# Kernel optimization log

Hardware: AMD Instinct MI355X
Metric: run time of the kernel (lower is better)

Reference implementation:

```python
import jax, jax.numpy as jnp
import numpy as np

HEADS = 16
EMBED = 1024
HEAD_DIM = EMBED // HEADS


def setup_inputs() -> dict:
    k = jax.random.key(0)
    ks = jax.random.split(k, 8)
    N, L = 8, 1024
    s = 1.0 / np.sqrt(HEAD_DIM)
    return {
        "key": jax.random.normal(ks[0], (N, L, EMBED), jnp.float32),
        "query": jax.random.normal(ks[1], (N, L, EMBED), jnp.float32),
        "value": jax.random.normal(ks[2], (N, L, EMBED), jnp.float32),
        "mask": jnp.ones((N, 1, 1, L), jnp.int32),
        "Wq": jax.random.normal(ks[3], (HEAD_DIM, HEAD_DIM), jnp.float32) * s,
        "Wk": jax.random.normal(ks[4], (HEAD_DIM, HEAD_DIM), jnp.float32) * s,
        "Wv": jax.random.normal(ks[5], (HEAD_DIM, HEAD_DIM), jnp.float32) * s,
        "Wo": jax.random.normal(ks[6], (EMBED, EMBED), jnp.float32) * (1.0 / np.sqrt(EMBED)),
    }


def reference(key, query, value, mask, Wq, Wk, Wv, Wo):
    # NOTE: original torch code calls weights.masked_fill(...) without assignment,
    # which is a no-op, so `mask` is faithfully ignored here.
    N, Lq, E = query.shape
    Lk = key.shape[1]
    H, D = HEADS, E // HEADS
    q = query.reshape(N, Lq, H, D)
    k = key.reshape(N, Lk, H, D)
    v = value.reshape(N, Lk, H, D)
    # per-head linear with weight shared across heads: x @ W^T (torch Linear)
    q = jnp.einsum('nqhd,ed->nqhe', q, Wq)
    k = jnp.einsum('nkhd,ed->nkhe', k, Wk)
    v = jnp.einsum('nkhd,ed->nkhe', v, Wv)
    weights = jnp.einsum('nqhd,nkhd->nhqk', q, k)
    attn = jax.nn.softmax(weights / jnp.sqrt(jnp.asarray(E, weights.dtype)), axis=-1)
    out = jnp.einsum('nhqk,nkhd->nqhd', attn, v).reshape(N, Lq, E)
    return out @ Wo.T
```

## Files before the change

kernel.cpp:

```cpp
#include <hip/hip_runtime.h>
#include <hip/hip_bf16.h>

#define HEADS 16
#define HDIM  64
#define EMB   1024
#define NB    8
#define SEQ   1024

typedef __bf16 bf16_t;
typedef __bf16 bf16x8 __attribute__((ext_vector_type(8)));
typedef __bf16 bf16x4 __attribute__((ext_vector_type(4)));
typedef float  floatx4 __attribute__((ext_vector_type(4)));
typedef float  f32x16  __attribute__((ext_vector_type(16)));
typedef unsigned uint2v __attribute__((ext_vector_type(2)));

union PkU { unsigned u; __bf16 h[2]; };
union W4U { unsigned u[4]; bf16x8 v; };

__device__ __forceinline__ bf16x8 load8bf(const bf16_t* p) { return *(const bf16x8*)p; }
__device__ __forceinline__ bf16x4 cvt4(float4 a) {
    bf16x4 r; r[0]=(bf16_t)a.x; r[1]=(bf16_t)a.y; r[2]=(bf16_t)a.z; r[3]=(bf16_t)a.w;
    return r;
}
__device__ __forceinline__ bf16x8 cvt8(float4 a, float4 b) {
    bf16x8 r;
    r[0]=(bf16_t)a.x; r[1]=(bf16_t)a.y; r[2]=(bf16_t)a.z; r[3]=(bf16_t)a.w;
    r[4]=(bf16_t)b.x; r[5]=(bf16_t)b.y; r[6]=(bf16_t)b.z; r[7]=(bf16_t)b.w;
    return r;
}

__global__ __launch_bounds__(256) void proj_kernel(
    const float* __restrict__ q_in, const float* __restrict__ k_in,
    const float* __restrict__ v_in,
    const float* __restrict__ Wq, const float* __restrict__ Wk,
    const float* __restrict__ Wv,
    bf16_t* __restrict__ qp, bf16_t* __restrict__ kp, bf16_t* __restrict__ vt)
{
    __shared__ __align__(16) bf16_t wl[64][72];
    __shared__ __align__(16) bf16_t lo[64][72];

    const int wave = threadIdx.x >> 6;
    const int lane = threadIdx.x & 63;
    const int m  = lane & 15;
    const int q4 = lane >> 4;
    const int op = blockIdx.y;

    const float* x = (op == 0) ? q_in : (op == 1) ? k_in : v_in;
    const float* W = (op == 0) ? Wq   : (op == 1) ? Wk   : Wv;

    {
        const int t  = threadIdx.x;
        const int f  = t >> 2;
        const int kg = (t & 3) * 16;
        #pragma unroll
        for (int j = 0; j < 4; ++j) {
            float4 v = *(const float4*)(W + f * 64 + kg + j * 4);
            *(bf16x4*)&wl[f][kg + j * 4] = cvt4(v);
        }
    }
    __syncthreads();

    if (op == 2) {
        const int nh = blockIdx.x >> 4;
        const int l0 = (blockIdx.x & 15) * 64;
        const int n  = nh >> 4;
        const int h  = nh & 15;

        const int la = l0 + wave * 16 + m;
        const float* xr = x + (size_t)(n * 16384 + la * 16 + h) * 64;
        float4 f0 = *(const float4*)(xr + q4 * 8);
        float4 f1 = *(const float4*)(xr + q4 * 8 + 4);
        float4 f2 = *(const float4*)(xr + 32 + q4 * 8);
        float4 f3 = *(const float4*)(xr + 32 + q4 * 8 + 4);
        bf16x8 a0 = cvt8(f0, f1);
        bf16x8 a1 = cvt8(f2, f3);

        floatx4 acc[4];
        #pragma unroll
        for (int sub = 0; sub < 4; ++sub) {
            bf16x8 b0 = load8bf(&wl[sub * 16 + m][q4 * 8]);
            bf16x8 b1 = load8bf(&wl[sub * 16 + m][32 + q4 * 8]);
            floatx4 z = {0.f, 0.f, 0.f, 0.f};
            z = __builtin_amdgcn_mfma_f32_16x16x32_bf16(a0, b0, z, 0, 0, 0);
            z = __builtin_amdgcn_mfma_f32_16x16x32_bf16(a1, b1, z, 0, 0, 0);
            acc[sub] = z;
        }

        #pragma unroll
        for (int sub = 0; sub < 4; ++sub) {
            #pragma unroll
            for (int r = 0; r < 4; r += 2) {
                PkU u; u.h[0] = (bf16_t)acc[sub][r]; u.h[1] = (bf16_t)acc[sub][r + 1];
                *(unsigned*)&lo[sub * 16 + m][wave * 16 + q4 * 4 + r] = u.u;
            }
        }
        __syncthreads();

        const int e  = threadIdx.x >> 2;
        const int lc = (threadIdx.x & 3) * 16;
        bf16_t* dst = vt + ((size_t)nh * 64 + e) * 1024 + l0 + lc;
        *(bf16x8*)dst       = *(const bf16x8*)&lo[e][lc];
        *(bf16x8*)(dst + 8) = *(const bf16x8*)&lo[e][lc + 8];
    } else {
        const float qscale = (op == 0) ? (1.4426950408889634f * 0.03125f) : 1.0f;
        const int row0 = blockIdx.x * 64 + wave * 16;

        const float* xr = x + (size_t)(row0 + m) * 64;
        float4 f0 = *(const float4*)(xr + q4 * 8);
        float4 f1 = *(const float4*)(xr + q4 * 8 + 4);
        float4 f2 = *(const float4*)(xr + 32 + q4 * 8);
        float4 f3 = *(const float4*)(xr + 32 + q4 * 8 + 4);
        bf16x8 a0 = cvt8(f0, f1);
        bf16x8 a1 = cvt8(f2, f3);

        floatx4 acc[4];
        #pragma unroll
        for (int sub = 0; sub < 4; ++sub) {
            bf16x8 b0 = load8bf(&wl[sub * 16 + m][q4 * 8]);
            bf16x8 b1 = load8bf(&wl[sub * 16 + m][32 + q4 * 8]);
            floatx4 z = {0.f, 0.f, 0.f, 0.f};
            z = __builtin_amdgcn_mfma_f32_16x16x32_bf16(a0, b0, z, 0, 0, 0);
            z = __builtin_amdgcn_mfma_f32_16x16x32_bf16(a1, b1, z, 0, 0, 0);
            acc[sub] = z;
        }

        #pragma unroll
        for (int sub = 0; sub < 4; ++sub) {
            #pragma unroll
            for (int r = 0; r < 4; ++r) {
                lo[wave * 16 + q4 * 4 + r][sub * 16 + m] = (bf16_t)(acc[sub][r] * qscale);
            }
        }
        __syncthreads();

        const int gl = threadIdx.x >> 2;
        const int ec = (threadIdx.x & 3) * 16;
        const int g  = blockIdx.x * 64 + gl;
        const int n  = g >> 14;
        const int l  = (g >> 4) & 1023;
        const int h  = g & 15;
        const int nh = n * 16 + h;
        bf16_t* dst = ((op == 0) ? qp : kp) + ((size_t)nh * 1024 + l) * 64 + ec;
        *(bf16x8*)dst       = *(const bf16x8*)&lo[gl][ec];
        *(bf16x8*)(dst + 8) = *(const bf16x8*)&lo[gl][ec + 8];
    }
}

__global__ __launch_bounds__(256) void attn_kernel(
    bf16_t* __restrict__ qp, const bf16_t* __restrict__ kp,
    const bf16_t* __restrict__ vt)
{
    __shared__ __align__(16) bf16_t kl[2][64][64];
    __shared__ __align__(16) bf16_t vl[2][64][64];

    const int lane = threadIdx.x & 63;
    const int wave = threadIdx.x >> 6;
    const int q32  = lane & 31;
    const int hi   = lane >> 5;

    const int nh   = blockIdx.x & 127;
    const int qblk = blockIdx.x >> 7;

    bf16_t* Q = qp + (size_t)nh * 65536;
    const bf16_t* K = kp + (size_t)nh * 65536;
    const bf16_t* V = vt + (size_t)nh * 65536;

    const int qb = qblk * 128 + wave * 32;

    const int srow  = lane >> 3;
    const int sslot = lane & 7;
    const int ch    = sslot ^ srow;

    auto stage = [&](int b, int kb) {
        #pragma unroll
        for (int i = 0; i < 2; ++i) {
            const int rbase = wave * 16 + i * 8;
            const int row   = rbase + srow;
            __builtin_amdgcn_global_load_lds(
                (const __attribute__((address_space(1))) unsigned int*)(K + (size_t)(kb + row) * 64 + ch * 8),
                (__attribute__((address_space(3))) unsigned int*)(&kl[b][rbase][0]),
                16, 0, 0);
            __builtin_amdgcn_global_load_lds(
                (const __attribute__((address_space(1))) unsigned int*)(V + (size_t)row * 1024 + kb + ch * 8),
                (__attribute__((address_space(3))) unsigned int*)(&vl[b][rbase][0]),
                16, 0, 0);
        }
    };

    stage(0, 0);

    bf16x8 bq[4];
    #pragma unroll
    for (int sl = 0; sl < 4; ++sl)
        bq[sl] = load8bf(Q + (size_t)(qb + q32) * 64 + sl * 16 + hi * 8);

    bf16x8 ones;
    #pragma unroll
    for (int j = 0; j < 8; ++j) ones[j] = (bf16_t)1.0f;

    f32x16 o0 = {0.f,0.f,0.f,0.f,0.f,0.f,0.f,0.f,0.f,0.f,0.f,0.f,0.f,0.f,0.f,0.f};
    f32x16 o1 = o0;
    f32x16 osum = o0;

    int cur = 0;
    __syncthreads();

    for (int kt = 0; kt < 16; ++kt) {
        if (kt < 15) stage(cur ^ 1, (kt + 1) * 64);

        #pragma unroll
        for (int kb32 = 0; kb32 < 2; ++kb32) {
            const int krow = kb32 * 32 + q32;
            f32x16 s = {0.f,0.f,0.f,0.f,0.f,0.f,0.f,0.f,0.f,0.f,0.f,0.f,0.f,0.f,0.f,0.f};
            __builtin_amdgcn_s_setprio(1);
            #pragma unroll
            for (int sl = 0; sl < 4; ++sl) {
                const int ck = ((sl * 2 + hi) ^ (krow & 7)) * 8;
                bf16x8 ka = load8bf(&kl[cur][krow][ck]);
                s = __builtin_amdgcn_mfma_f32_32x32x16_bf16(ka, bq[sl], s, 0, 0, 0);
            }
            __builtin_amdgcn_s_setprio(0);

            unsigned w[8];
            #pragma unroll
            for (int t = 0; t < 8; ++t) {
                float p0 = exp2f(s[2 * t]);
                float p1 = exp2f(s[2 * t + 1]);
                PkU u; u.h[0] = (bf16_t)p0; u.h[1] = (bf16_t)p1;
                w[t] = u.u;
            }

            bf16x8 va[4];
            #pragma unroll
            for (int db = 0; db < 2; ++db) {
                const int d = db * 32 + q32;
                #pragma unroll
                for (int c = 0; c < 2; ++c) {
                    const int cv = ((kb32 * 4 + c * 2 + hi) ^ (d & 7)) * 8;
                    va[db * 2 + c] = load8bf(&vl[cur][d][cv]);
                }
            }

            W4U b0v, b1v;
            uint2v r02 = __builtin_amdgcn_permlane32_swap(w[0], w[2], false, false);
            b0v.u[0] = r02[0]; b0v.u[2] = r02[1];
            uint2v r13 = __builtin_amdgcn_permlane32_swap(w[1], w[3], false, false);
            b0v.u[1] = r13[0]; b0v.u[3] = r13[1];
            uint2v r46 = __builtin_amdgcn_permlane32_swap(w[4], w[6], false, false);
            b1v.u[0] = r46[0]; b1v.u[2] = r46[1];
            uint2v r57 = __builtin_amdgcn_permlane32_swap(w[5], w[7], false, false);
            b1v.u[1] = r57[0]; b1v.u[3] = r57[1];

            __builtin_amdgcn_s_setprio(1);
            o0 = __builtin_amdgcn_mfma_f32_32x32x16_bf16(va[0], b0v.v, o0, 0, 0, 0);
            o0 = __builtin_amdgcn_mfma_f32_32x32x16_bf16(va[1], b1v.v, o0, 0, 0, 0);
            o1 = __builtin_amdgcn_mfma_f32_32x32x16_bf16(va[2], b0v.v, o1, 0, 0, 0);
            o1 = __builtin_amdgcn_mfma_f32_32x32x16_bf16(va[3], b1v.v, o1, 0, 0, 0);
            osum = __builtin_amdgcn_mfma_f32_32x32x16_bf16(ones, b0v.v, osum, 0, 0, 0);
            osum = __builtin_amdgcn_mfma_f32_32x32x16_bf16(ones, b1v.v, osum, 0, 0, 0);
            __builtin_amdgcn_s_setprio(0);
        }

        __syncthreads();
        cur ^= 1;
    }

    const float inv = 1.0f / osum[0];

    #pragma unroll
    for (int g = 0; g < 4; ++g) {
        bf16x4 w0v, w1v;
        #pragma unroll
        for (int r = 0; r < 4; ++r) {
            w0v[r] = (bf16_t)(o0[g * 4 + r] * inv);
            w1v[r] = (bf16_t)(o1[g * 4 + r] * inv);
        }
        *(bf16x4*)(Q + (size_t)(qb + q32) * 64 +      g * 8 + hi * 4) = w0v;
        *(bf16x4*)(Q + (size_t)(qb + q32) * 64 + 32 + g * 8 + hi * 4) = w1v;
    }
}

__global__ __launch_bounds__(256) void wocvt_kernel(
    const float* __restrict__ Wo, bf16_t* __restrict__ wo_bf)
{
    const int i = (blockIdx.x * 256 + threadIdx.x) * 8;
    float4 f0 = *(const float4*)(Wo + i);
    float4 f1 = *(const float4*)(Wo + i + 4);
    *(bf16x8*)(wo_bf + i) = cvt8(f0, f1);
}

__global__ __launch_bounds__(256) void outproj_kernel(
    const bf16_t* __restrict__ aoq, const bf16_t* __restrict__ wo_bf,
    float* __restrict__ out)
{
    __shared__ __align__(16) bf16_t wl[64][72];

    const int wave = threadIdx.x >> 6;
    const int lane = threadIdx.x & 63;
    const int m  = lane & 15;
    const int q4 = lane >> 4;

    const int by = blockIdx.x & 15;
    const int bx = blockIdx.x >> 4;

    const int row0 = bx * 128 + wave * 32;
    const int col0 = by * 64;

    const int ts_f  = threadIdx.x >> 2;
    const int ts_kg = (threadIdx.x & 3) * 16;

    floatx4 acc[2][4];
    #pragma unroll
    for (int rs = 0; rs < 2; ++rs)
        #pragma unroll
        for (int cs = 0; cs < 4; ++cs) acc[rs][cs] = (floatx4){0.f, 0.f, 0.f, 0.f};

    for (int h = 0; h < 16; ++h) {
        const int kc = h * 64;
        __syncthreads();
        *(bf16x8*)&wl[ts_f][ts_kg] =
            load8bf(wo_bf + (size_t)(col0 + ts_f) * 1024 + kc + ts_kg);
        *(bf16x8*)&wl[ts_f][ts_kg + 8] =
            load8bf(wo_bf + (size_t)(col0 + ts_f) * 1024 + kc + ts_kg + 8);
        __syncthreads();

        bf16x8 a[2][2];
        #pragma unroll
        for (int rs = 0; rs < 2; ++rs) {
            const int g = row0 + rs * 16 + m;
            const int n = g >> 10;
            const int q = g & 1023;
            const bf16_t* arow = aoq + ((size_t)(n * 16 + h) * 1024 + q) * 64;
            a[rs][0] = load8bf(arow + q4 * 8);
            a[rs][1] = load8bf(arow + 32 + q4 * 8);
        }

        #pragma unroll
        for (int cs = 0; cs < 4; ++cs) {
            bf16x8 b0 = load8bf(&wl[cs * 16 + m][q4 * 8]);
            bf16x8 b1 = load8bf(&wl[cs * 16 + m][32 + q4 * 8]);
            #pragma unroll
            for (int rs = 0; rs < 2; ++rs) {
                acc[rs][cs] = __builtin_amdgcn_mfma_f32_16x16x32_bf16(a[rs][0], b0, acc[rs][cs], 0, 0, 0);
                acc[rs][cs] = __builtin_amdgcn_mfma_f32_16x16x32_bf16(a[rs][1], b1, acc[rs][cs], 0, 0, 0);
            }
        }
    }

    #pragma unroll
    for (int rs = 0; rs < 2; ++rs) {
        #pragma unroll
        for (int r = 0; r < 4; ++r) {
            const int g = row0 + rs * 16 + q4 * 4 + r;
            #pragma unroll
            for (int cs = 0; cs < 4; ++cs)
                out[(size_t)g * 1024 + col0 + cs * 16 + m] = acc[rs][cs][r];
        }
    }
}

extern "C" void kernel_launch(void* const* d_in, const int* in_sizes, int n_in,
                              void* d_out, int out_size, void* d_ws, size_t ws_size,
                              hipStream_t stream) {
    const float* key   = (const float*)d_in[0];
    const float* query = (const float*)d_in[1];
    const float* value = (const float*)d_in[2];
    const float* Wq = (const float*)d_in[4];
    const float* Wk = (const float*)d_in[5];
    const float* Wv = (const float*)d_in[6];
    const float* Wo = (const float*)d_in[7];

    const size_t TENS = (size_t)NB * SEQ * EMB;
    bf16_t* qp = (bf16_t*)d_ws;
    bf16_t* vt = qp + TENS;
    bf16_t* kp = (bf16_t*)d_out;

    hipLaunchKernelGGL(proj_kernel, dim3(2048, 3), dim3(256), 0, stream,
                       query, key, value, Wq, Wk, Wv, qp, kp, vt);
    hipLaunchKernelGGL(attn_kernel, dim3(1024), dim3(256), 0, stream, qp, kp, vt);
    hipLaunchKernelGGL(wocvt_kernel, dim3(512), dim3(256), 0, stream, Wo, vt);
    hipLaunchKernelGGL(outproj_kernel, dim3(1024), dim3(256), 0, stream,
                       qp, vt, (float*)d_out);
}
```

Before: 257.2 us.

## Process four tiles per projection block and fuse Wo conversion into outproj

The projection kernel now loops over four 64-row tiles per block, with double-buffered output staging, so the weight conversion into shared memory is amortized and the grid shrinks fourfold. The separate Wo fp32-to-bf16 conversion kernel is removed, and outproj reads fp32 Wo directly and converts it while loading shared memory. This saves one launch and the bf16 Wo round trip. In exchange, outproj reads twice the bytes for Wo, repeated across row blocks, and the projection has less parallelism per launch.

```diff
diff --git a/kernel.cpp b/kernel.cpp
--- a/kernel.cpp
+++ b/kernel.cpp
@@ -37,7 +37,7 @@
     bf16_t* __restrict__ qp, bf16_t* __restrict__ kp, bf16_t* __restrict__ vt)
 {
     __shared__ __align__(16) bf16_t wl[64][72];
-    __shared__ __align__(16) bf16_t lo[64][72];
+    __shared__ __align__(16) bf16_t lo[2][64][72];
 
     const int wave = threadIdx.x >> 6;
     const int lane = threadIdx.x & 63;
@@ -60,89 +60,95 @@
     }
     __syncthreads();
 
-    if (op == 2) {
-        const int nh = blockIdx.x >> 4;
-        const int l0 = (blockIdx.x & 15) * 64;
-        const int n  = nh >> 4;
-        const int h  = nh & 15;
-
-        const int la = l0 + wave * 16 + m;
-        const float* xr = x + (size_t)(n * 16384 + la * 16 + h) * 64;
-        float4 f0 = *(const float4*)(xr + q4 * 8);
-        float4 f1 = *(const float4*)(xr + q4 * 8 + 4);
-        float4 f2 = *(const float4*)(xr + 32 + q4 * 8);
-        float4 f3 = *(const float4*)(xr + 32 + q4 * 8 + 4);
-        bf16x8 a0 = cvt8(f0, f1);
-        bf16x8 a1 = cvt8(f2, f3);
-
-        floatx4 acc[4];
-        #pragma unroll
-        for (int sub = 0; sub < 4; ++sub) {
-            bf16x8 b0 = load8bf(&wl[sub * 16 + m][q4 * 8]);
-            bf16x8 b1 = load8bf(&wl[sub * 16 + m][32 + q4 * 8]);
-            floatx4 z = {0.f, 0.f, 0.f, 0.f};
-            z = __builtin_amdgcn_mfma_f32_16x16x32_bf16(a0, b0, z, 0, 0, 0);
-            z = __builtin_amdgcn_mfma_f32_16x16x32_bf16(a1, b1, z, 0, 0, 0);
-            acc[sub] = z;
-        }
-
-        #pragma unroll
-        for (int sub = 0; sub < 4; ++sub) {
-            #pragma unroll
-            for (int r = 0; r < 4; r += 2) {
-                PkU u; u.h[0] = (bf16_t)acc[sub][r]; u.h[1] = (bf16_t)acc[sub][r + 1];
-                *(unsigned*)&lo[sub * 16 + m][wave * 16 + q4 * 4 + r] = u.u;
-            }
-        }
-        __syncthreads();
-
-        const int e  = threadIdx.x >> 2;
-        const int lc = (threadIdx.x & 3) * 16;
-        bf16_t* dst = vt + ((size_t)nh * 64 + e) * 1024 + l0 + lc;
-        *(bf16x8*)dst       = *(const bf16x8*)&lo[e][lc];
-        *(bf16x8*)(dst + 8) = *(const bf16x8*)&lo[e][lc + 8];
-    } else {
-        const float qscale = (op == 0) ? (1.4426950408889634f * 0.03125f) : 1.0f;
-        const int row0 = blockIdx.x * 64 + wave * 16;
-
-        const float* xr = x + (size_t)(row0 + m) * 64;
-        float4 f0 = *(const float4*)(xr + q4 * 8);
-        float4 f1 = *(const float4*)(xr + q4 * 8 + 4);
-        float4 f2 = *(const float4*)(xr + 32 + q4 * 8);
-        float4 f3 = *(const float4*)(xr + 32 + q4 * 8 + 4);
-        bf16x8 a0 = cvt8(f0, f1);
-        bf16x8 a1 = cvt8(f2, f3);
-
-        floatx4 acc[4];
-        #pragma unroll
-        for (int sub = 0; sub < 4; ++sub) {
-            bf16x8 b0 = load8bf(&wl[sub * 16 + m][q4 * 8]);
-            bf16x8 b1 = load8bf(&wl[sub * 16 + m][32 + q4 * 8]);
-            floatx4 z = {0.f, 0.f, 0.f, 0.f};
-            z = __builtin_amdgcn_mfma_f32_16x16x32_bf16(a0, b0, z, 0, 0, 0);
-            z = __builtin_amdgcn_mfma_f32_16x16x32_bf16(a1, b1, z, 0, 0, 0);
-            acc[sub] = z;
-        }
-
-        #pragma unroll
-        for (int sub = 0; sub < 4; ++sub) {
-            #pragma unroll
-            for (int r = 0; r < 4; ++r) {
-                lo[wave * 16 + q4 * 4 + r][sub * 16 + m] = (bf16_t)(acc[sub][r] * qscale);
-            }
-        }
-        __syncthreads();
-
-        const int gl = threadIdx.x >> 2;
-        const int ec = (threadIdx.x & 3) * 16;
-        const int g  = blockIdx.x * 64 + gl;
-        const int n  = g >> 14;
-        const int l  = (g >> 4) & 1023;
-        const int h  = g & 15;
-        const int nh = n * 16 + h;
-        bf16_t* dst = ((op == 0) ? qp : kp) + ((size_t)nh * 1024 + l) * 64 + ec;
-        *(bf16x8*)dst       = *(const bf16x8*)&lo[gl][ec];
-        *(bf16x8*)(dst + 8) = *(const bf16x8*)&lo[gl][ec + 8];
+    #pragma unroll 1
+    for (int i = 0; i < 4; ++i) {
+        const int tile = blockIdx.x * 4 + i;
+        const int buf  = i & 1;
+
+        if (op == 2) {
+            const int nh = tile >> 4;
+            const int l0 = (tile & 15) * 64;
+            const int n  = nh >> 4;
+            const int h  = nh & 15;
+
+            const int la = l0 + wave * 16 + m;
+            const float* xr = x + (size_t)(n * 16384 + la * 16 + h) * 64;
+            float4 f0 = *(const float4*)(xr + q4 * 8);
+            float4 f1 = *(const float4*)(xr + q4 * 8 + 4);
+            float4 f2 = *(const float4*)(xr + 32 + q4 * 8);
+            float4 f3 = *(const float4*)(xr + 32 + q4 * 8 + 4);
+            bf16x8 a0 = cvt8(f0, f1);
+            bf16x8 a1 = cvt8(f2, f3);
+
+            floatx4 acc[4];
+            #pragma unroll
+            for (int sub = 0; sub < 4; ++sub) {
+                bf16x8 b0 = load8bf(&wl[sub * 16 + m][q4 * 8]);
+                bf16x8 b1 = load8bf(&wl[sub * 16 + m][32 + q4 * 8]);
+                floatx4 z = {0.f, 0.f, 0.f, 0.f};
+                z = __builtin_amdgcn_mfma_f32_16x16x32_bf16(a0, b0, z, 0, 0, 0);
+                z = __builtin_amdgcn_mfma_f32_16x16x32_bf16(a1, b1, z, 0, 0, 0);
+                acc[sub] = z;
+            }
+
+            #pragma unroll
+            for (int sub = 0; sub < 4; ++sub) {
+                #pragma unroll
+                for (int r = 0; r < 4; r += 2) {
+                    PkU u; u.h[0] = (bf16_t)acc[sub][r]; u.h[1] = (bf16_t)acc[sub][r + 1];
+                    *(unsigned*)&lo[buf][sub * 16 + m][wave * 16 + q4 * 4 + r] = u.u;
+                }
+            }
+            __syncthreads();
+
+            const int e  = threadIdx.x >> 2;
+            const int lc = (threadIdx.x & 3) * 16;
+            bf16_t* dst = vt + ((size_t)nh * 64 + e) * 1024 + l0 + lc;
+            *(bf16x8*)dst       = *(const bf16x8*)&lo[buf][e][lc];
+            *(bf16x8*)(dst + 8) = *(const bf16x8*)&lo[buf][e][lc + 8];
+        } else {
+            const float qscale = (op == 0) ? (1.4426950408889634f * 0.03125f) : 1.0f;
+            const int row0 = tile * 64 + wave * 16;
+
+            const float* xr = x + (size_t)(row0 + m) * 64;
+            float4 f0 = *(const float4*)(xr + q4 * 8);
+            float4 f1 = *(const float4*)(xr + q4 * 8 + 4);
+            float4 f2 = *(const float4*)(xr + 32 + q4 * 8);
+            float4 f3 = *(const float4*)(xr + 32 + q4 * 8 + 4);
+            bf16x8 a0 = cvt8(f0, f1);
+            bf16x8 a1 = cvt8(f2, f3);
+
+            floatx4 acc[4];
+            #pragma unroll
+            for (int sub = 0; sub < 4; ++sub) {
+                bf16x8 b0 = load8bf(&wl[sub * 16 + m][q4 * 8]);
+                bf16x8 b1 = load8bf(&wl[sub * 16 + m][32 + q4 * 8]);
+                floatx4 z = {0.f, 0.f, 0.f, 0.f};
+                z = __builtin_amdgcn_mfma_f32_16x16x32_bf16(a0, b0, z, 0, 0, 0);
+                z = __builtin_amdgcn_mfma_f32_16x16x32_bf16(a1, b1, z, 0, 0, 0);
+                acc[sub] = z;
+            }
+
+            #pragma unroll
+            for (int sub = 0; sub < 4; ++sub) {
+                #pragma unroll
+                for (int r = 0; r < 4; ++r) {
+                    lo[buf][wave * 16 + q4 * 4 + r][sub * 16 + m] = (bf16_t)(acc[sub][r] * qscale);
+                }
+            }
+            __syncthreads();
+
+            const int gl = threadIdx.x >> 2;
+            const int ec = (threadIdx.x & 3) * 16;
+            const int g  = tile * 64 + gl;
+            const int n  = g >> 14;
+            const int l  = (g >> 4) & 1023;
+            const int h  = g & 15;
+            const int nh = n * 16 + h;
+            bf16_t* dst = ((op == 0) ? qp : kp) + ((size_t)nh * 1024 + l) * 64 + ec;
+            *(bf16x8*)dst       = *(const bf16x8*)&lo[buf][gl][ec];
+            *(bf16x8*)(dst + 8) = *(const bf16x8*)&lo[buf][gl][ec + 8];
+        }
     }
 }
 
@@ -280,17 +286,8 @@
     }
 }
 
-__global__ __launch_bounds__(256) void wocvt_kernel(
-    const float* __restrict__ Wo, bf16_t* __restrict__ wo_bf)
-{
-    const int i = (blockIdx.x * 256 + threadIdx.x) * 8;
-    float4 f0 = *(const float4*)(Wo + i);
-    float4 f1 = *(const float4*)(Wo + i + 4);
-    *(bf16x8*)(wo_bf + i) = cvt8(f0, f1);
-}
-
 __global__ __launch_bounds__(256) void outproj_kernel(
-    const bf16_t* __restrict__ aoq, const bf16_t* __restrict__ wo_bf,
+    const bf16_t* __restrict__ aoq, const float* __restrict__ Wo,
     float* __restrict__ out)
 {
     __shared__ __align__(16) bf16_t wl[64][72];
@@ -318,10 +315,15 @@
     for (int h = 0; h < 16; ++h) {
         const int kc = h * 64;
         __syncthreads();
-        *(bf16x8*)&wl[ts_f][ts_kg] =
-            load8bf(wo_bf + (size_t)(col0 + ts_f) * 1024 + kc + ts_kg);
-        *(bf16x8*)&wl[ts_f][ts_kg + 8] =
-            load8bf(wo_bf + (size_t)(col0 + ts_f) * 1024 + kc + ts_kg + 8);
+        {
+            const float* wrow = Wo + (size_t)(col0 + ts_f) * 1024 + kc + ts_kg;
+            float4 w0 = *(const float4*)(wrow);
+            float4 w1 = *(const float4*)(wrow + 4);
+            float4 w2 = *(const float4*)(wrow + 8);
+            float4 w3 = *(const float4*)(wrow + 12);
+            *(bf16x8*)&wl[ts_f][ts_kg]     = cvt8(w0, w1);
+            *(bf16x8*)&wl[ts_f][ts_kg + 8] = cvt8(w2, w3);
+        }
         __syncthreads();
 
         bf16x8 a[2][2];
@@ -375,10 +377,9 @@
     bf16_t* vt = qp + TENS;
     bf16_t* kp = (bf16_t*)d_out;
 
-    hipLaunchKernelGGL(proj_kernel, dim3(2048, 3), dim3(256), 0, stream,
+    hipLaunchKernelGGL(proj_kernel, dim3(512, 3), dim3(256), 0, stream,
                        query, key, value, Wq, Wk, Wv, qp, kp, vt);
     hipLaunchKernelGGL(attn_kernel, dim3(1024), dim3(256), 0, stream, qp, kp, vt);
-    hipLaunchKernelGGL(wocvt_kernel, dim3(512), dim3(256), 0, stream, Wo, vt);
     hipLaunchKernelGGL(outproj_kernel, dim3(1024), dim3(256), 0, stream,
-                       qp, vt, (float*)d_out);
-}
+                       qp, Wo, (float*)d_out);
+}
```

After: 264.1 us. 2.7% more time.

## Double-buffer Wo tiles in outproj via async global_load_lds with XOR swizzle

Applied to the files above, without the earlier changes.

The output projection kernel now double-buffers the Wo tile in shared memory and fills it with direct global-to-LDS loads, issued one head ahead of the MFMA loop. It drops the padded layout in favour of an XOR-swizzled 64x64 layout to avoid bank conflicts, and it cuts the two barriers per iteration down to one. This targets load latency and barrier stalls in the out-projection, which is one kernel of several. The risk lies in whether the single barrier correctly orders the asynchronous LDS writes against the reads of the next iteration.

```diff
diff --git a/kernel.cpp b/kernel.cpp
--- a/kernel.cpp
+++ b/kernel.cpp
@@ -293,7 +293,7 @@
     const bf16_t* __restrict__ aoq, const bf16_t* __restrict__ wo_bf,
     float* __restrict__ out)
 {
-    __shared__ __align__(16) bf16_t wl[64][72];
+    __shared__ __align__(16) bf16_t wl[2][64][64];
 
     const int wave = threadIdx.x >> 6;
     const int lane = threadIdx.x & 63;
@@ -306,8 +306,26 @@
     const int row0 = bx * 128 + wave * 32;
     const int col0 = by * 64;
 
-    const int ts_f  = threadIdx.x >> 2;
-    const int ts_kg = (threadIdx.x & 3) * 16;
+    const int srow  = lane >> 3;
+    const int sslot = lane & 7;
+    const int ch    = sslot ^ srow;
+
+    auto stage = [&](int b, int h) {
+        #pragma unroll
+        for (int i = 0; i < 2; ++i) {
+            const int rbase = wave * 16 + i * 8;
+            const int row   = rbase + srow;
+            __builtin_amdgcn_global_load_lds(
+                (const __attribute__((address_space(1))) unsigned int*)(wo_bf + (size_t)(col0 + row) * 1024 + h * 64 + ch * 8),
+                (__attribute__((address_space(3))) unsigned int*)(&wl[b][rbase][0]),
+                16, 0, 0);
+        }
+    };
+
+    const int c0 = (q4 ^ (m & 7)) * 8;
+    const int c1 = ((q4 + 4) ^ (m & 7)) * 8;
+
+    stage(0, 0);
 
     floatx4 acc[2][4];
     #pragma unroll
@@ -315,15 +333,10 @@
         #pragma unroll
         for (int cs = 0; cs < 4; ++cs) acc[rs][cs] = (floatx4){0.f, 0.f, 0.f, 0.f};
 
+    int cur = 0;
+    __syncthreads();
+
     for (int h = 0; h < 16; ++h) {
-        const int kc = h * 64;
-        __syncthreads();
-        *(bf16x8*)&wl[ts_f][ts_kg] =
-            load8bf(wo_bf + (size_t)(col0 + ts_f) * 1024 + kc + ts_kg);
-        *(bf16x8*)&wl[ts_f][ts_kg + 8] =
-            load8bf(wo_bf + (size_t)(col0 + ts_f) * 1024 + kc + ts_kg + 8);
-        __syncthreads();
-
         bf16x8 a[2][2];
         #pragma unroll
         for (int rs = 0; rs < 2; ++rs) {
@@ -335,16 +348,22 @@
             a[rs][1] = load8bf(arow + 32 + q4 * 8);
         }
 
+        if (h < 15) stage(cur ^ 1, h + 1);
+
         #pragma unroll
         for (int cs = 0; cs < 4; ++cs) {
-            bf16x8 b0 = load8bf(&wl[cs * 16 + m][q4 * 8]);
-            bf16x8 b1 = load8bf(&wl[cs * 16 + m][32 + q4 * 8]);
+            const int rr = cs * 16 + m;
+            bf16x8 b0 = load8bf(&wl[cur][rr][c0]);
+            bf16x8 b1 = load8bf(&wl[cur][rr][c1]);
             #pragma unroll
             for (int rs = 0; rs < 2; ++rs) {
                 acc[rs][cs] = __builtin_amdgcn_mfma_f32_16x16x32_bf16(a[rs][0], b0, acc[rs][cs], 0, 0, 0);
                 acc[rs][cs] = __builtin_amdgcn_mfma_f32_16x16x32_bf16(a[rs][1], b1, acc[rs][cs], 0, 0, 0);
             }
         }
+
+        __syncthreads();
+        cur ^= 1;
     }
 
     #pragma unroll
```

Measured after the change: 257.1 us. About the same (-0.0%).
